# Kernel tuning notes

Measured on AMD Instinct MI355X. Metric: run time of the kernel, lower is better.

Reference implementation:

```python
import jax, jax.numpy as jnp
import numpy as np

TOPK = 2


def setup_inputs() -> dict:
    key = jax.random.key(0)
    k1, k2 = jax.random.split(key)
    B, N, D, E, C = 4, 2048, 2048, 8, 512
    token_inputs = jax.random.normal(k1, (B, N, D), dtype=jnp.float32)
    # bottleneck_in.weight.t() stacked over experts: [E, D, C]; scaled like a real init
    bottleneck_weights = jax.random.normal(k2, (E, D, C), dtype=jnp.float32) * 0.02
    return {
        "token_inputs": token_inputs,
        "bottleneck_weights": bottleneck_weights,
        "expert_capacity": 640,
    }


def _routing(router_probs, expert_capacity, topk):
    # router_probs: [B, N, E]
    B, N, E = router_probs.shape
    _, expert_indices = jax.lax.top_k(router_probs, topk)      # [B, N, topk]
    idx = jnp.transpose(expert_indices, (0, 2, 1)).reshape(B, topk * N)
    expert_mask = jax.nn.one_hot(idx, E, dtype=jnp.int32)       # [B, topk*N, E]
    token_priority = jnp.cumsum(expert_mask, axis=1) * expert_mask - 1
    token_priority = token_priority.reshape(B, topk, N, E)
    token_priority = jnp.transpose(token_priority, (0, 2, 1, 3))  # [B, N, topk, E]
    token_priority = jnp.max(token_priority, axis=2)              # [B, N, E]
    # one-hot over capacity; negative (-1) and >= capacity priorities map to all-zero rows
    cap_range = jnp.arange(expert_capacity, dtype=jnp.int32)
    dispatch = (token_priority[..., None] == cap_range).astype(jnp.float32)  # [B,N,E,C]
    combine = router_probs[..., None] * dispatch                            # [B,N,E,C]
    return dispatch, combine


def reference(token_inputs, bottleneck_weights, expert_capacity):
    # activation_cache: [B, N, E, Cb]
    activation_cache = jnp.einsum("bnd,edc->bnec", token_inputs, bottleneck_weights)
    router_logits = jnp.sqrt(jnp.sum(activation_cache * activation_cache, axis=-1))  # [B,N,E]
    router_probs = jax.nn.softmax(router_logits, axis=-1)
    dispatch, combine = _routing(router_probs, expert_capacity, TOPK)
    return jnp.stack([dispatch, combine], axis=0)  # [2, B, N, E, capacity]
```

## Files before the change

kernel.cpp:

```cpp
#include <hip/hip_runtime.h>
#include <math.h>

constexpr int Bb = 4, Nn = 2048, Dd = 2048, Ee = 8, Cbn = 512;
constexpr int Mm = Bb * Nn;

typedef _Float16 half8 __attribute__((ext_vector_type(8)));
typedef float floatx16 __attribute__((ext_vector_type(16)));

#define GLL16(g, l)                                                     \
  __builtin_amdgcn_global_load_lds(                                     \
      (const __attribute__((address_space(1))) void*)(g),               \
      (__attribute__((address_space(3))) void*)(l), 16, 0, 0)

__global__ __launch_bounds__(256) void split_x(const float* __restrict__ X,
                                               _Float16* __restrict__ hi,
                                               _Float16* __restrict__ lo) {
  const int i = (blockIdx.x * 256 + threadIdx.x) * 8;
  float4 v0 = *(const float4*)(X + i);
  float4 v1 = *(const float4*)(X + i + 4);
  half8 h, l;
  h[0] = (_Float16)v0.x; l[0] = (_Float16)(v0.x - (float)h[0]);
  h[1] = (_Float16)v0.y; l[1] = (_Float16)(v0.y - (float)h[1]);
  h[2] = (_Float16)v0.z; l[2] = (_Float16)(v0.z - (float)h[2]);
  h[3] = (_Float16)v0.w; l[3] = (_Float16)(v0.w - (float)h[3]);
  h[4] = (_Float16)v1.x; l[4] = (_Float16)(v1.x - (float)h[4]);
  h[5] = (_Float16)v1.y; l[5] = (_Float16)(v1.y - (float)h[5]);
  h[6] = (_Float16)v1.z; l[6] = (_Float16)(v1.z - (float)h[6]);
  h[7] = (_Float16)v1.w; l[7] = (_Float16)(v1.w - (float)h[7]);
  *(half8*)(hi + i) = h;
  *(half8*)(lo + i) = l;
}

__global__ __launch_bounds__(256) void transpose_w(const float* __restrict__ W,
                                                   _Float16* __restrict__ WThi,
                                                   _Float16* __restrict__ WTlo) {
  const int kt = blockIdx.x;
  const int ct = blockIdx.y;
  const int e = blockIdx.z;
  __shared__ _Float16 thi[64][72];
  __shared__ _Float16 tlo[64][72];
  const int tx = threadIdx.x & 15, ty = threadIdx.x >> 4;
  const float* src = W + ((size_t)(e * 2048 + kt * 64)) * 512 + ct * 64;
#pragma unroll
  for (int p = 0; p < 4; ++p) {
    int kk = ty + p * 16;
    float4 v = *(const float4*)(src + (size_t)kk * 512 + tx * 4);
    _Float16 h;
    h = (_Float16)v.x; thi[tx * 4 + 0][kk] = h; tlo[tx * 4 + 0][kk] = (_Float16)(v.x - (float)h);
    h = (_Float16)v.y; thi[tx * 4 + 1][kk] = h; tlo[tx * 4 + 1][kk] = (_Float16)(v.y - (float)h);
    h = (_Float16)v.z; thi[tx * 4 + 2][kk] = h; tlo[tx * 4 + 2][kk] = (_Float16)(v.z - (float)h);
    h = (_Float16)v.w; thi[tx * 4 + 3][kk] = h; tlo[tx * 4 + 3][kk] = (_Float16)(v.w - (float)h);
  }
  __syncthreads();
  const int rr = threadIdx.x >> 3;
  const int ch = threadIdx.x & 7;
  _Float16* dh = WThi + ((size_t)(e * 512 + ct * 64)) * 2048 + kt * 64;
  _Float16* dl = WTlo + ((size_t)(e * 512 + ct * 64)) * 2048 + kt * 64;
#pragma unroll
  for (int p = 0; p < 2; ++p) {
    int cc = rr + p * 32;
    *(half8*)(dh + (size_t)cc * 2048 + ch * 8) = *(const half8*)(&thi[cc][ch * 8]);
    *(half8*)(dl + (size_t)cc * 2048 + ch * 8) = *(const half8*)(&tlo[cc][ch * 8]);
  }
}

__global__ __launch_bounds__(256) void gemm_mfma(const _Float16* __restrict__ Xhi,
                                                 const _Float16* __restrict__ Xlo,
                                                 const _Float16* __restrict__ WThi,
                                                 const _Float16* __restrict__ WTlo,
                                                 float* __restrict__ partial) {
  const int bid = blockIdx.x;
  const int st = bid >> 8;
  const int stm = st & 3;
  const int stn = st >> 2;
  const int li = bid & 255;
  const int mtile = stm * 16 + (li >> 4);
  const int ntile = stn * 16 + (li & 15);

  const int tid = threadIdx.x;
  const int wave = tid >> 6, lane = tid & 63;
  const int wm = wave >> 1, wn = wave & 1;
  const int h = lane >> 5;

  __shared__ __align__(16) char lds[32768];
  char* ldsAhi = lds;
  char* ldsAlo = lds + 8192;
  char* ldsBhi = lds + 16384;
  char* ldsBlo = lds + 24576;

  const int lr = lane >> 2;
  const int cpos = lane & 3;
  const int cg = cpos ^ ((lr >> 1) & 3);
  const int r0 = wave * 32 + lr;
  const int r1 = r0 + 16;
  const _Float16* xh0 = Xhi + (size_t)(mtile * 128 + r0) * 2048 + cg * 8;
  const _Float16* xh1 = Xhi + (size_t)(mtile * 128 + r1) * 2048 + cg * 8;
  const _Float16* xl0 = Xlo + (size_t)(mtile * 128 + r0) * 2048 + cg * 8;
  const _Float16* xl1 = Xlo + (size_t)(mtile * 128 + r1) * 2048 + cg * 8;
  const _Float16* wh0 = WThi + (size_t)(ntile * 128 + r0) * 2048 + cg * 8;
  const _Float16* wh1 = WThi + (size_t)(ntile * 128 + r1) * 2048 + cg * 8;
  const _Float16* wl0 = WTlo + (size_t)(ntile * 128 + r0) * 2048 + cg * 8;
  const _Float16* wl1 = WTlo + (size_t)(ntile * 128 + r1) * 2048 + cg * 8;
  const int lq0 = wave * 2048;
  const int lq1 = lq0 + 1024;

  const int rA0 = wm * 64 + (lane & 31);
  const int rA1 = rA0 + 32;
  const int rB0 = wn * 64 + (lane & 31);
  const int rB1 = rB0 + 32;
  auto foff = [&](int r, int s) {
    return r * 64 + (((s * 2 + h) ^ ((r >> 1) & 3)) << 4);
  };
  const int oA0[2] = {foff(rA0, 0), foff(rA0, 1)};
  const int oA1[2] = {foff(rA1, 0), foff(rA1, 1)};
  const int oB0[2] = {foff(rB0, 0), foff(rB0, 1)};
  const int oB1[2] = {foff(rB1, 0), foff(rB1, 1)};

  floatx16 acc00 = {}, acc01 = {}, acc10 = {}, acc11 = {};

  for (int kt = 0; kt < 64; ++kt) {
    const int k0 = kt * 32;
    GLL16(xh0 + k0, ldsAhi + lq0);
    GLL16(xh1 + k0, ldsAhi + lq1);
    GLL16(xl0 + k0, ldsAlo + lq0);
    GLL16(xl1 + k0, ldsAlo + lq1);
    GLL16(wh0 + k0, ldsBhi + lq0);
    GLL16(wh1 + k0, ldsBhi + lq1);
    GLL16(wl0 + k0, ldsBlo + lq0);
    GLL16(wl1 + k0, ldsBlo + lq1);
    __syncthreads();
#pragma unroll
    for (int s = 0; s < 2; ++s) {
      half8 ah0 = *(const half8*)(ldsAhi + oA0[s]);
      half8 ah1 = *(const half8*)(ldsAhi + oA1[s]);
      half8 al0 = *(const half8*)(ldsAlo + oA0[s]);
      half8 al1 = *(const half8*)(ldsAlo + oA1[s]);
      half8 bh0 = *(const half8*)(ldsBhi + oB0[s]);
      half8 bh1 = *(const half8*)(ldsBhi + oB1[s]);
      half8 bl0 = *(const half8*)(ldsBlo + oB0[s]);
      half8 bl1 = *(const half8*)(ldsBlo + oB1[s]);
      acc00 = __builtin_amdgcn_mfma_f32_32x32x16_f16(ah0, bh0, acc00, 0, 0, 0);
      acc00 = __builtin_amdgcn_mfma_f32_32x32x16_f16(ah0, bl0, acc00, 0, 0, 0);
      acc00 = __builtin_amdgcn_mfma_f32_32x32x16_f16(al0, bh0, acc00, 0, 0, 0);
      acc01 = __builtin_amdgcn_mfma_f32_32x32x16_f16(ah0, bh1, acc01, 0, 0, 0);
      acc01 = __builtin_amdgcn_mfma_f32_32x32x16_f16(ah0, bl1, acc01, 0, 0, 0);
      acc01 = __builtin_amdgcn_mfma_f32_32x32x16_f16(al0, bh1, acc01, 0, 0, 0);
      acc10 = __builtin_amdgcn_mfma_f32_32x32x16_f16(ah1, bh0, acc10, 0, 0, 0);
      acc10 = __builtin_amdgcn_mfma_f32_32x32x16_f16(ah1, bl0, acc10, 0, 0, 0);
      acc10 = __builtin_amdgcn_mfma_f32_32x32x16_f16(al1, bh0, acc10, 0, 0, 0);
      acc11 = __builtin_amdgcn_mfma_f32_32x32x16_f16(ah1, bh1, acc11, 0, 0, 0);
      acc11 = __builtin_amdgcn_mfma_f32_32x32x16_f16(ah1, bl1, acc11, 0, 0, 0);
      acc11 = __builtin_amdgcn_mfma_f32_32x32x16_f16(al1, bh1, acc11, 0, 0, 0);
    }
    __syncthreads();
  }

  float myv = 0.f;
#pragma unroll
  for (int i = 0; i < 2; ++i) {
    const floatx16& c0 = i ? acc10 : acc00;
    const floatx16& c1 = i ? acc11 : acc01;
#pragma unroll
    for (int reg = 0; reg < 16; ++reg) {
      float v = c0[reg] * c0[reg] + c1[reg] * c1[reg];
#pragma unroll
      for (int m = 1; m <= 16; m <<= 1) v += __shfl_xor(v, m, 64);
      if ((lane & 31) == i * 16 + reg) myv = v;
    }
  }
  {
    const int i = (lane & 31) >> 4;
    const int reg = lane & 15;
    const int row = i * 32 + (reg & 3) + 8 * (reg >> 2) + 4 * h;
    const int token = mtile * 128 + wm * 64 + row;
    const int slice = ntile * 2 + wn;
    partial[(size_t)slice * Mm + token] = myv;
  }
}

__global__ void route_kernel(const float* __restrict__ partial,
                             int* __restrict__ idx1, int* __restrict__ idx2,
                             float* __restrict__ p1, float* __restrict__ p2) {
  int t = blockIdx.x * blockDim.x + threadIdx.x;
  if (t >= Mm) return;
  float l[Ee];
  float mx = -1e30f;
#pragma unroll
  for (int e = 0; e < Ee; ++e) {
    float s = 0.f;
#pragma unroll
    for (int u = 0; u < 8; ++u) s += partial[(size_t)(e * 8 + u) * Mm + t];
    l[e] = sqrtf(s);
    mx = fmaxf(mx, l[e]);
  }
  float p[Ee];
  float s = 0.f;
#pragma unroll
  for (int e = 0; e < Ee; ++e) {
    p[e] = expf(l[e] - mx);
    s += p[e];
  }
  float inv = 1.f / s;
  int i1 = 0;
  float b1 = l[0];
#pragma unroll
  for (int e = 1; e < Ee; ++e)
    if (l[e] > b1) { b1 = l[e]; i1 = e; }
  int i2 = -1;
  float b2 = -1e30f;
#pragma unroll
  for (int e = 0; e < Ee; ++e)
    if (e != i1 && l[e] > b2) { b2 = l[e]; i2 = e; }
  idx1[t] = i1;
  idx2[t] = i2;
  p1[t] = p[i1] * inv;
  p2[t] = p[i2] * inv;
}

__global__ void scan_kernel(const int* __restrict__ idx1,
                            const int* __restrict__ idx2,
                            int* __restrict__ prios) {
  const int b = blockIdx.x;
  const int tid = threadIdx.x;
  __shared__ int cnts[256][8];
  int cnt[8] = {0, 0, 0, 0, 0, 0, 0, 0};
  int eloc[16];
  const int base_p = tid * 16;
#pragma unroll
  for (int i = 0; i < 16; ++i) {
    int p = base_p + i;
    int k = p >> 11;
    int n = p & (Nn - 1);
    int e = (k == 0 ? idx1 : idx2)[b * Nn + n];
    eloc[i] = e;
    cnt[e]++;
  }
#pragma unroll
  for (int e = 0; e < 8; ++e) cnts[tid][e] = cnt[e];
  __syncthreads();
  if (tid < 8) {
    int run = 0;
    for (int i = 0; i < 256; ++i) {
      int v = cnts[i][tid];
      cnts[i][tid] = run;
      run += v;
    }
  }
  __syncthreads();
  int base[8];
#pragma unroll
  for (int e = 0; e < 8; ++e) base[e] = cnts[tid][e];
#pragma unroll
  for (int i = 0; i < 16; ++i) {
    int e = eloc[i];
    prios[b * 2 * Nn + base_p + i] = base[e]++;
  }
}

__global__ void zero_kernel(float4* __restrict__ out, int n4) {
  int i = blockIdx.x * blockDim.x + threadIdx.x;
  if (i < n4) out[i] = make_float4(0.f, 0.f, 0.f, 0.f);
}

__global__ void scatter_kernel(const int* __restrict__ idx1,
                               const int* __restrict__ idx2,
                               const float* __restrict__ p1,
                               const float* __restrict__ p2,
                               const int* __restrict__ prios,
                               float* __restrict__ out, int cap) {
  int t = blockIdx.x * blockDim.x + threadIdx.x;
  if (t >= Mm) return;
  int b = t >> 11;
  int n = t & (Nn - 1);
  size_t disp = (size_t)t * Ee * cap;
  size_t comb = disp + (size_t)Mm * Ee * cap;
  {
    int e = idx1[t];
    int p = prios[b * 2 * Nn + n];
    if (p < cap) {
      out[disp + (size_t)e * cap + p] = 1.f;
      out[comb + (size_t)e * cap + p] = p1[t];
    }
  }
  {
    int e = idx2[t];
    int p = prios[b * 2 * Nn + Nn + n];
    if (p < cap) {
      out[disp + (size_t)e * cap + p] = 1.f;
      out[comb + (size_t)e * cap + p] = p2[t];
    }
  }
}

extern "C" void kernel_launch(void* const* d_in, const int* in_sizes, int n_in,
                              void* d_out, int out_size, void* d_ws, size_t ws_size,
                              hipStream_t stream) {
  const float* X = (const float*)d_in[0];
  const float* W = (const float*)d_in[1];
  float* out = (float*)d_out;
  const int cap = out_size / (2 * Bb * Nn * Ee);

  char* ws = (char*)d_ws;
  _Float16* Xhi = (_Float16*)ws;
  _Float16* Xlo = (_Float16*)(ws + 33554432ull);
  _Float16* WThi = (_Float16*)(ws + 67108864ull);
  _Float16* WTlo = (_Float16*)(ws + 83886080ull);
  float* partial = (float*)(ws + 100663296ull);
  int* idx1 = (int*)(ws + 102760448ull);
  int* idx2 = idx1 + Mm;
  float* p1 = (float*)(idx2 + Mm);
  float* p2 = p1 + Mm;
  int* prios = (int*)(p2 + Mm);

  split_x<<<(Mm * Dd) / 2048, 256, 0, stream>>>(X, Xhi, Xlo);
  transpose_w<<<dim3(32, 8, 8), 256, 0, stream>>>(W, WThi, WTlo);
  gemm_mfma<<<2048, 256, 0, stream>>>(Xhi, Xlo, WThi, WTlo, partial);
  route_kernel<<<Mm / 256, 256, 0, stream>>>(partial, idx1, idx2, p1, p2);
  scan_kernel<<<Bb, 256, 0, stream>>>(idx1, idx2, prios);
  const int n4 = out_size / 4;
  zero_kernel<<<(n4 + 255) / 256, 256, 0, stream>>>((float4*)out, n4);
  scatter_kernel<<<Mm / 256, 256, 0, stream>>>(idx1, idx2, p1, p2, prios, out, cap);
}
```

Measured before the change: 818.9 us.

## Fuse X fp16 hi/lo split into GEMM, loading fp32 X tiles directly

Removes the separate split_x pass, which read 64MB of fp32 X and wrote 64MB of fp16 hi/lo arrays. The GEMM now streams fp32 X tiles into LDS with a new XOR swizzle and converts them to hi/lo fp16 fragments in registers before the MFMAs. The partial-sums layout also changes to token-major so the route kernel reads contiguously. The trade-off is more conversion ALU work inside the GEMM inner loop, repeated for every N tile that reuses the same X rows, and fp32 A tiles read per block equal in size to the old hi+lo pair.

```diff
diff --git a/kernel.cpp b/kernel.cpp
--- a/kernel.cpp
+++ b/kernel.cpp
@@ -11,25 +11,6 @@
   __builtin_amdgcn_global_load_lds(                                     \
       (const __attribute__((address_space(1))) void*)(g),               \
       (__attribute__((address_space(3))) void*)(l), 16, 0, 0)
-
-__global__ __launch_bounds__(256) void split_x(const float* __restrict__ X,
-                                               _Float16* __restrict__ hi,
-                                               _Float16* __restrict__ lo) {
-  const int i = (blockIdx.x * 256 + threadIdx.x) * 8;
-  float4 v0 = *(const float4*)(X + i);
-  float4 v1 = *(const float4*)(X + i + 4);
-  half8 h, l;
-  h[0] = (_Float16)v0.x; l[0] = (_Float16)(v0.x - (float)h[0]);
-  h[1] = (_Float16)v0.y; l[1] = (_Float16)(v0.y - (float)h[1]);
-  h[2] = (_Float16)v0.z; l[2] = (_Float16)(v0.z - (float)h[2]);
-  h[3] = (_Float16)v0.w; l[3] = (_Float16)(v0.w - (float)h[3]);
-  h[4] = (_Float16)v1.x; l[4] = (_Float16)(v1.x - (float)h[4]);
-  h[5] = (_Float16)v1.y; l[5] = (_Float16)(v1.y - (float)h[5]);
-  h[6] = (_Float16)v1.z; l[6] = (_Float16)(v1.z - (float)h[6]);
-  h[7] = (_Float16)v1.w; l[7] = (_Float16)(v1.w - (float)h[7]);
-  *(half8*)(hi + i) = h;
-  *(half8*)(lo + i) = l;
-}
 
 __global__ __launch_bounds__(256) void transpose_w(const float* __restrict__ W,
                                                    _Float16* __restrict__ WThi,
@@ -64,8 +45,7 @@
   }
 }
 
-__global__ __launch_bounds__(256) void gemm_mfma(const _Float16* __restrict__ Xhi,
-                                                 const _Float16* __restrict__ Xlo,
+__global__ __launch_bounds__(256) void gemm_mfma(const float* __restrict__ X,
                                                  const _Float16* __restrict__ WThi,
                                                  const _Float16* __restrict__ WTlo,
                                                  float* __restrict__ partial) {
@@ -83,58 +63,83 @@
   const int h = lane >> 5;
 
   __shared__ __align__(16) char lds[32768];
-  char* ldsAhi = lds;
-  char* ldsAlo = lds + 8192;
+  char* ldsA = lds;
   char* ldsBhi = lds + 16384;
   char* ldsBlo = lds + 24576;
 
-  const int lr = lane >> 2;
-  const int cpos = lane & 3;
-  const int cg = cpos ^ ((lr >> 1) & 3);
-  const int r0 = wave * 32 + lr;
-  const int r1 = r0 + 16;
-  const _Float16* xh0 = Xhi + (size_t)(mtile * 128 + r0) * 2048 + cg * 8;
-  const _Float16* xh1 = Xhi + (size_t)(mtile * 128 + r1) * 2048 + cg * 8;
-  const _Float16* xl0 = Xlo + (size_t)(mtile * 128 + r0) * 2048 + cg * 8;
-  const _Float16* xl1 = Xlo + (size_t)(mtile * 128 + r1) * 2048 + cg * 8;
-  const _Float16* wh0 = WThi + (size_t)(ntile * 128 + r0) * 2048 + cg * 8;
-  const _Float16* wh1 = WThi + (size_t)(ntile * 128 + r1) * 2048 + cg * 8;
-  const _Float16* wl0 = WTlo + (size_t)(ntile * 128 + r0) * 2048 + cg * 8;
-  const _Float16* wl1 = WTlo + (size_t)(ntile * 128 + r1) * 2048 + cg * 8;
-  const int lq0 = wave * 2048;
-  const int lq1 = lq0 + 1024;
-
-  const int rA0 = wm * 64 + (lane & 31);
-  const int rA1 = rA0 + 32;
+  const int lrA = lane >> 3;
+  const int cposA = lane & 7;
+  const int cgA = cposA ^ lrA;
+  const float* xg[4];
+  int ldsAoff[4];
+#pragma unroll
+  for (int q = 0; q < 4; ++q) {
+    const int row = wave * 32 + q * 8 + lrA;
+    xg[q] = X + (size_t)(mtile * 128 + row) * 2048 + cgA * 4;
+    ldsAoff[q] = (wave * 32 + q * 8) * 128;
+  }
+
+  const int lrB = lane >> 2;
+  const int cposB = lane & 3;
+  const int cgB = cposB ^ ((lrB >> 1) & 3);
+  const int rB0s = wave * 32 + lrB;
+  const int rB1s = rB0s + 16;
+  const _Float16* wh0 = WThi + (size_t)(ntile * 128 + rB0s) * 2048 + cgB * 8;
+  const _Float16* wh1 = WThi + (size_t)(ntile * 128 + rB1s) * 2048 + cgB * 8;
+  const _Float16* wl0 = WTlo + (size_t)(ntile * 128 + rB0s) * 2048 + cgB * 8;
+  const _Float16* wl1 = WTlo + (size_t)(ntile * 128 + rB1s) * 2048 + cgB * 8;
+  const int lqB0 = wave * 2048;
+  const int lqB1 = lqB0 + 1024;
+
+  const int keyA = lane & 7;
+  const int rowA0 = wm * 64 + (lane & 31);
+  const int rowA1 = rowA0 + 32;
+  int oAf0[2][2], oAf1[2][2];
+#pragma unroll
+  for (int s = 0; s < 2; ++s)
+#pragma unroll
+    for (int c = 0; c < 2; ++c) {
+      const int g = s * 4 + h * 2 + c;
+      oAf0[s][c] = rowA0 * 128 + ((g ^ keyA) << 4);
+      oAf1[s][c] = rowA1 * 128 + ((g ^ keyA) << 4);
+    }
+
   const int rB0 = wn * 64 + (lane & 31);
   const int rB1 = rB0 + 32;
-  auto foff = [&](int r, int s) {
+  auto foffB = [&](int r, int s) {
     return r * 64 + (((s * 2 + h) ^ ((r >> 1) & 3)) << 4);
   };
-  const int oA0[2] = {foff(rA0, 0), foff(rA0, 1)};
-  const int oA1[2] = {foff(rA1, 0), foff(rA1, 1)};
-  const int oB0[2] = {foff(rB0, 0), foff(rB0, 1)};
-  const int oB1[2] = {foff(rB1, 0), foff(rB1, 1)};
+  const int oB0[2] = {foffB(rB0, 0), foffB(rB0, 1)};
+  const int oB1[2] = {foffB(rB1, 0), foffB(rB1, 1)};
 
   floatx16 acc00 = {}, acc01 = {}, acc10 = {}, acc11 = {};
+
+  auto cvtA = [](const char* p0, const char* p1, half8& ah, half8& al) {
+    float4 f0 = *(const float4*)p0;
+    float4 f1 = *(const float4*)p1;
+    float xf[8] = {f0.x, f0.y, f0.z, f0.w, f1.x, f1.y, f1.z, f1.w};
+#pragma unroll
+    for (int j = 0; j < 8; ++j) {
+      _Float16 hv = (_Float16)xf[j];
+      ah[j] = hv;
+      al[j] = (_Float16)(xf[j] - (float)hv);
+    }
+  };
 
   for (int kt = 0; kt < 64; ++kt) {
     const int k0 = kt * 32;
-    GLL16(xh0 + k0, ldsAhi + lq0);
-    GLL16(xh1 + k0, ldsAhi + lq1);
-    GLL16(xl0 + k0, ldsAlo + lq0);
-    GLL16(xl1 + k0, ldsAlo + lq1);
-    GLL16(wh0 + k0, ldsBhi + lq0);
-    GLL16(wh1 + k0, ldsBhi + lq1);
-    GLL16(wl0 + k0, ldsBlo + lq0);
-    GLL16(wl1 + k0, ldsBlo + lq1);
+#pragma unroll
+    for (int q = 0; q < 4; ++q) GLL16(xg[q] + k0, ldsA + ldsAoff[q]);
+    GLL16(wh0 + k0, ldsBhi + lqB0);
+    GLL16(wh1 + k0, ldsBhi + lqB1);
+    GLL16(wl0 + k0, ldsBlo + lqB0);
+    GLL16(wl1 + k0, ldsBlo + lqB1);
     __syncthreads();
 #pragma unroll
     for (int s = 0; s < 2; ++s) {
-      half8 ah0 = *(const half8*)(ldsAhi + oA0[s]);
-      half8 ah1 = *(const half8*)(ldsAhi + oA1[s]);
-      half8 al0 = *(const half8*)(ldsAlo + oA0[s]);
-      half8 al1 = *(const half8*)(ldsAlo + oA1[s]);
+      half8 ah0, al0, ah1, al1;
+      cvtA(ldsA + oAf0[s][0], ldsA + oAf0[s][1], ah0, al0);
+      cvtA(ldsA + oAf1[s][0], ldsA + oAf1[s][1], ah1, al1);
       half8 bh0 = *(const half8*)(ldsBhi + oB0[s]);
       half8 bh1 = *(const half8*)(ldsBhi + oB1[s]);
       half8 bl0 = *(const half8*)(ldsBlo + oB0[s]);
@@ -174,7 +179,7 @@
     const int row = i * 32 + (reg & 3) + 8 * (reg >> 2) + 4 * h;
     const int token = mtile * 128 + wm * 64 + row;
     const int slice = ntile * 2 + wn;
-    partial[(size_t)slice * Mm + token] = myv;
+    partial[(size_t)token * 64 + slice] = myv;
   }
 }
 
@@ -189,7 +194,7 @@
   for (int e = 0; e < Ee; ++e) {
     float s = 0.f;
 #pragma unroll
-    for (int u = 0; u < 8; ++u) s += partial[(size_t)(e * 8 + u) * Mm + t];
+    for (int u = 0; u < 8; ++u) s += partial[(size_t)t * 64 + e * 8 + u];
     l[e] = sqrtf(s);
     mx = fmaxf(mx, l[e]);
   }
@@ -301,20 +306,17 @@
   const int cap = out_size / (2 * Bb * Nn * Ee);
 
   char* ws = (char*)d_ws;
-  _Float16* Xhi = (_Float16*)ws;
-  _Float16* Xlo = (_Float16*)(ws + 33554432ull);
-  _Float16* WThi = (_Float16*)(ws + 67108864ull);
-  _Float16* WTlo = (_Float16*)(ws + 83886080ull);
-  float* partial = (float*)(ws + 100663296ull);
-  int* idx1 = (int*)(ws + 102760448ull);
+  _Float16* WThi = (_Float16*)ws;
+  _Float16* WTlo = (_Float16*)(ws + 16777216ull);
+  float* partial = (float*)(ws + 33554432ull);
+  int* idx1 = (int*)(ws + 35651584ull);
   int* idx2 = idx1 + Mm;
   float* p1 = (float*)(idx2 + Mm);
   float* p2 = p1 + Mm;
   int* prios = (int*)(p2 + Mm);
 
-  split_x<<<(Mm * Dd) / 2048, 256, 0, stream>>>(X, Xhi, Xlo);
   transpose_w<<<dim3(32, 8, 8), 256, 0, stream>>>(W, WThi, WTlo);
-  gemm_mfma<<<2048, 256, 0, stream>>>(Xhi, Xlo, WThi, WTlo, partial);
+  gemm_mfma<<<2048, 256, 0, stream>>>(X, WThi, WTlo, partial);
   route_kernel<<<Mm / 256, 256, 0, stream>>>(partial, idx1, idx2, p1, p2);
   scan_kernel<<<Bb, 256, 0, stream>>>(idx1, idx2, prios);
   const int n4 = out_size / 4;
```

Measured after the change: 808.9 us. About the same (-1.2%).
